# Kernel optimization log

Hardware: AMD Instinct MI355X
Metric: run time of the kernel (lower is better)

The kernel has to match this reference:

```python
import jax, jax.numpy as jnp
import numpy as np

QLEN, MLEN, D, H = 1024, 1024, 1024, 16
DH = D // H
KLEN = QLEN + MLEN
SCALE = 1.0 / np.sqrt(DH).astype(np.float32)
W_STD = 0.02


def setup_inputs() -> dict:
    key = jax.random.key(0)
    ks = jax.random.split(key, 14)
    inputs = jax.random.normal(ks[0], (QLEN, 1, D), jnp.float32)
    r = jax.random.normal(ks[1], (KLEN, D), jnp.float32)
    u = jax.random.normal(ks[2], (H, DH), jnp.float32) * W_STD
    v = jax.random.normal(ks[3], (H, DH), jnp.float32) * W_STD
    mem = jax.random.normal(ks[4], (MLEN, 1, D), jnp.float32)
    # causal mask over concatenated [mem, inputs] keys: True = masked
    attn_mask = jnp.triu(jnp.ones((QLEN, KLEN), bool), k=MLEN + 1)
    W_qkv = jax.random.normal(ks[5], (3 * D, D), jnp.float32) * W_STD
    W_r = jax.random.normal(ks[6], (D, D), jnp.float32) * W_STD
    W_o = jax.random.normal(ks[7], (D, D), jnp.float32) * W_STD
    W_ih = jax.random.normal(ks[8], (3 * D, D), jnp.float32) * W_STD
    W_hh = jax.random.normal(ks[9], (3 * D, D), jnp.float32) * W_STD
    b_ih = jnp.zeros((3 * D,), jnp.float32)
    b_hh = jnp.zeros((3 * D,), jnp.float32)
    h0 = jnp.zeros((1, 1, D), jnp.float32)  # GRU hidden, forces batch=1
    return {"inputs": inputs, "r": r, "u": u, "v": v, "attn_mask": attn_mask,
            "mem": mem, "W_qkv": W_qkv, "W_r": W_r, "W_o": W_o,
            "W_ih": W_ih, "W_hh": W_hh, "b_ih": b_ih, "b_hh": b_hh, "h0": h0}


def _rel_shift(x):
    # Transformer-XL relative shift; x: [qlen, klen, b, n]
    q, k, b, n = x.shape
    zp = jnp.zeros((q, 1, b, n), x.dtype)
    xp = jnp.concatenate([zp, x], axis=1)          # [q, k+1, b, n]
    xp = xp.reshape(k + 1, q, b, n)[1:]            # drop first row
    return xp.reshape(q, k, b, n)


def reference(inputs, r, u, v, attn_mask, mem, W_qkv, W_r, W_o,
              W_ih, W_hh, b_ih, b_hh, h0):
    qlen, b, d = inputs.shape
    cat = jnp.concatenate([mem, inputs], axis=0)        # [klen, b, d]
    klen = cat.shape[0]
    w_heads = cat @ W_qkv.T                             # [klen, b, 3d]
    q_h, k_h, v_h = jnp.split(w_heads, 3, axis=-1)
    q_h = q_h[-qlen:].reshape(qlen, b, H, DH)
    k_h = k_h.reshape(klen, b, H, DH)
    v_h = v_h.reshape(klen, b, H, DH)
    r_k = (r @ W_r.T).reshape(klen, H, DH)              # relative key heads

    AC = jnp.einsum('ibnd,jbnd->ijbn', q_h + u, k_h)    # content score
    BD = _rel_shift(jnp.einsum('ibnd,jnd->ijbn', q_h + v, r_k))  # position score
    score = (AC + BD) * SCALE                           # [q, k, b, n]
    score = jnp.where(attn_mask[:, :, None, None], jnp.float32(-1e30), score)
    probs = jax.nn.softmax(score, axis=1)

    attn_vec = jnp.einsum('ijbn,jbnd->ibnd', probs, v_h).reshape(qlen, b, d)
    y = attn_vec @ W_o.T                                # [q, b, d]

    # 1-layer GRU over time (PyTorch gate order r, z, n)
    x_proj = y @ W_ih.T + b_ih                          # [q, b, 3d]

    def step(h, xt):
        gh = h @ W_hh.T + b_hh
        xr, xz, xn = jnp.split(xt, 3, axis=-1)
        hr, hz, hn = jnp.split(gh, 3, axis=-1)
        rg = jax.nn.sigmoid(xr + hr)
        zg = jax.nn.sigmoid(xz + hz)
        ng = jnp.tanh(xn + rg * hn)
        h_new = (1.0 - zg) * ng + zg * h
        return h_new, h_new

    _, ys = jax.lax.scan(step, h0[0], x_proj)           # h0[0]: [b, d]
    return ys, probs
```

## Files before the change

### kernel.cpp

```cpp
#include <hip/hip_runtime.h>
#include <hip/hip_bf16.h>
#include <math.h>

#define QL   1024
#define ML   1024
#define KL   2048
#define DM   1024
#define NH   16
#define DH   64
#define SCL  0.125f
#define GRU_BLOCKS 128
#define GRU_ELPB   8

typedef __attribute__((ext_vector_type(8))) short bfrag;
typedef __attribute__((ext_vector_type(4))) float facc;

static __device__ __forceinline__ float dot4(const float4& a, const float4& b) {
    return a.x*b.x + a.y*b.y + a.z*b.z + a.w*b.w;
}

static __device__ __forceinline__ unsigned bf16_rne(float x) {
    unsigned u = __float_as_uint(x);
    return (u + 0x7FFF + ((u >> 16) & 1)) >> 16;
}
static __device__ __forceinline__ void bfsplit(float a, short& h, short& l) {
    unsigned uh = bf16_rne(a);
    h = (short)uh;
    float ah = __uint_as_float(uh << 16);
    l = (short)bf16_rne(a - ah);
}

__global__ __launch_bounds__(256) void gemm_nt_mfma(
    const float* __restrict__ A, const float* __restrict__ B,
    const float* __restrict__ bias, float* __restrict__ C,
    int M, int N, int K, int skipM, int skipN)
{
    const int bx = blockIdx.x, by = blockIdx.y;
    if (by < skipM && bx < skipN) return;
    __shared__ short Ah[128*40], Al[128*40], Bh[128*40], Bl[128*40];
    const int tid = threadIdx.x;
    const int wv = tid >> 6, ln = tid & 63;
    const int wr = wv >> 1, wc = wv & 1;
    const int lm = ln & 15, lk = ln >> 4;
    facc acc[4][4] = {};

    const int srow = tid >> 1;
    const int scol = (tid & 1) << 4;
    const float* Ap = A + (size_t)(by*128 + srow)*K + scol;
    const float* Bp = B + (size_t)(bx*128 + srow)*K + scol;

    float4 ar[4], br[4];
    #pragma unroll
    for (int c = 0; c < 4; c++) {
        ar[c] = *(const float4*)(Ap + c*4);
        br[c] = *(const float4*)(Bp + c*4);
    }

    for (int k0 = 0; k0 < K; k0 += 32) {
        bfrag a_h0, a_h1, a_l0, a_l1, b_h0, b_h1, b_l0, b_l1;
        #pragma unroll
        for (int c = 0; c < 4; c++) {
            const float av[4] = {ar[c].x, ar[c].y, ar[c].z, ar[c].w};
            const float bv[4] = {br[c].x, br[c].y, br[c].z, br[c].w};
            #pragma unroll
            for (int q = 0; q < 4; q++) {
                const int e = c*4 + q;
                short h, l;
                bfsplit(av[q], h, l);
                if (e < 8) { a_h0[e] = h; a_l0[e] = l; }
                else       { a_h1[e-8] = h; a_l1[e-8] = l; }
                bfsplit(bv[q], h, l);
                if (e < 8) { b_h0[e] = h; b_l0[e] = l; }
                else       { b_h1[e-8] = h; b_l1[e-8] = l; }
            }
        }
        __syncthreads();
        *(bfrag*)&Ah[srow*40 + scol    ] = a_h0;
        *(bfrag*)&Ah[srow*40 + scol + 8] = a_h1;
        *(bfrag*)&Al[srow*40 + scol    ] = a_l0;
        *(bfrag*)&Al[srow*40 + scol + 8] = a_l1;
        *(bfrag*)&Bh[srow*40 + scol    ] = b_h0;
        *(bfrag*)&Bh[srow*40 + scol + 8] = b_h1;
        *(bfrag*)&Bl[srow*40 + scol    ] = b_l0;
        *(bfrag*)&Bl[srow*40 + scol + 8] = b_l1;
        __syncthreads();
        if (k0 + 32 < K) {
            #pragma unroll
            for (int c = 0; c < 4; c++) {
                ar[c] = *(const float4*)(Ap + k0 + 32 + c*4);
                br[c] = *(const float4*)(Bp + k0 + 32 + c*4);
            }
        }
        bfrag fah[4], fal[4], fbh[4], fbl[4];
        #pragma unroll
        for (int i = 0; i < 4; i++) {
            const int rA = wr*64 + i*16 + lm;
            fah[i] = *(const bfrag*)&Ah[rA*40 + lk*8];
            fal[i] = *(const bfrag*)&Al[rA*40 + lk*8];
            const int rB = wc*64 + i*16 + lm;
            fbh[i] = *(const bfrag*)&Bh[rB*40 + lk*8];
            fbl[i] = *(const bfrag*)&Bl[rB*40 + lk*8];
        }
        #pragma unroll
        for (int i = 0; i < 4; i++)
            #pragma unroll
            for (int j = 0; j < 4; j++) {
                acc[i][j] = __builtin_amdgcn_mfma_f32_16x16x32_bf16(fah[i], fbh[j], acc[i][j], 0, 0, 0);
                acc[i][j] = __builtin_amdgcn_mfma_f32_16x16x32_bf16(fah[i], fbl[j], acc[i][j], 0, 0, 0);
                acc[i][j] = __builtin_amdgcn_mfma_f32_16x16x32_bf16(fal[i], fbh[j], acc[i][j], 0, 0, 0);
            }
    }

    const int m0 = by*128 + wr*64 + lk*4;
    const int n0 = bx*128 + wc*64 + lm;
    #pragma unroll
    for (int j = 0; j < 4; j++) {
        const float bj = bias ? bias[n0 + j*16] : 0.f;
        #pragma unroll
        for (int i = 0; i < 4; i++)
            #pragma unroll
            for (int r = 0; r < 4; r++)
                C[(size_t)(m0 + i*16 + r)*N + n0 + j*16] = acc[i][j][r] + bj;
    }
}

__global__ __launch_bounds__(256) void wd_kernel(
    const float* __restrict__ rk, const float* __restrict__ u_,
    const float* __restrict__ v_, float* __restrict__ wd)
{
    int idx = blockIdx.x*256 + threadIdx.x;
    if (idx >= NH*KL) return;
    int n = idx >> 11, jr = idx & (KL-1);
    const float* rp = rk + (size_t)jr*DM + n*DH;
    const float* up = u_ + n*DH;
    const float* vp = v_ + n*DH;
    float s = 0.f;
    #pragma unroll
    for (int d4 = 0; d4 < 16; d4++) {
        float4 r4 = *(const float4*)(rp + d4*4);
        float4 uu = *(const float4*)(up + d4*4);
        float4 vv = *(const float4*)(vp + d4*4);
        s += (vv.x-uu.x)*r4.x + (vv.y-uu.y)*r4.y + (vv.z-uu.z)*r4.z + (vv.w-uu.w)*r4.w;
    }
    wd[idx] = s;
}

__global__ __launch_bounds__(256) void score_kernel(
    const float* __restrict__ wh, const float* __restrict__ rk,
    const float* __restrict__ u_, const float* __restrict__ wd,
    float* __restrict__ sc)
{
    const int jt = blockIdx.x, it = blockIdx.y, n = blockIdx.z;
    const int i0 = it*64, j0 = jt*64;
    if (j0 > i0 + 1087) return;
    __shared__ float squ[64*64];
    __shared__ float sk [64*64];
    __shared__ float sr [128*64];
    __shared__ float swd[128];
    const int tid = threadIdx.x;
    #pragma unroll
    for (int rr = 0; rr < 4; rr++) {
        int p = tid + 256*rr;
        int row = p >> 4, c4 = p & 15;
        int phys = (c4 ^ ((row >> 2) & 15)) << 2;
        float4 q4 = *(const float4*)&wh[(size_t)(ML + i0 + row)*3072 + n*DH + (c4<<2)];
        float4 u4 = *(const float4*)&u_[n*DH + (c4<<2)];
        float4 t4; t4.x=q4.x+u4.x; t4.y=q4.y+u4.y; t4.z=q4.z+u4.z; t4.w=q4.w+u4.w;
        *(float4*)&squ[row*64 + phys] = t4;
        float4 k4 = *(const float4*)&wh[(size_t)(j0 + row)*3072 + DM + n*DH + (c4<<2)];
        *(float4*)&sk[row*64 + phys] = k4;
    }
    const int jr0 = j0 - i0 + 960;
    #pragma unroll
    for (int rr = 0; rr < 8; rr++) {
        int p = tid + 256*rr;
        int row = p >> 4, c4 = p & 15;
        int phys = (c4 ^ ((row >> 2) & 15)) << 2;
        int jr = jr0 + row;
        float4 r4;
        if (jr >= 0 && jr < KL) r4 = *(const float4*)&rk[(size_t)jr*DM + n*DH + (c4<<2)];
        else { r4.x = r4.y = r4.z = r4.w = 0.f; }
        *(float4*)&sr[row*64 + phys] = r4;
    }
    if (tid < 128) {
        int jr = jr0 + tid;
        swd[tid] = (jr >= 0 && jr < KL) ? wd[n*KL + jr] : 0.f;
    }
    __syncthreads();

    const int tj2 = tid & 15, ti2 = tid >> 4;
    const int rbase = tj2*4 - ti2*4 + 60;
    float acc[4][4] = {};
    #pragma unroll
    for (int dc = 0; dc < 16; dc++) {
        float4 qa[4], kb[4], rv[7];
        #pragma unroll
        for (int a = 0; a < 4; a++) {
            int row = ti2*4 + a;
            qa[a] = *(const float4*)&squ[row*64 + ((dc ^ ((row>>2)&15)) << 2)];
        }
        #pragma unroll
        for (int b_ = 0; b_ < 4; b_++) {
            int row = tj2*4 + b_;
            kb[b_] = *(const float4*)&sk[row*64 + ((dc ^ ((row>>2)&15)) << 2)];
        }
        #pragma unroll
        for (int o = 0; o < 7; o++) {
            int row = rbase + o;
            rv[o] = *(const float4*)&sr[row*64 + ((dc ^ ((row>>2)&15)) << 2)];
        }
        #pragma unroll
        for (int a = 0; a < 4; a++)
            #pragma unroll
            for (int b_ = 0; b_ < 4; b_++)
                acc[a][b_] += dot4(qa[a], kb[b_]) + dot4(qa[a], rv[3 + b_ - a]);
    }
    #pragma unroll
    for (int a = 0; a < 4; a++) {
        int i = i0 + ti2*4 + a;
        float4 o;
        o.x = (acc[a][0] + swd[rbase + 3 + 0 - a]) * SCL;
        o.y = (acc[a][1] + swd[rbase + 3 + 1 - a]) * SCL;
        o.z = (acc[a][2] + swd[rbase + 3 + 2 - a]) * SCL;
        o.w = (acc[a][3] + swd[rbase + 3 + 3 - a]) * SCL;
        *(float4*)&sc[((size_t)i*NH + n)*KL + j0 + (tj2<<2)] = o;
    }
}

__global__ __launch_bounds__(512) void softmaxT_kernel(float* __restrict__ sc)
{
    const int i = blockIdx.x;
    const int tid = threadIdx.x;
    __shared__ float ld[16*2052];
    __shared__ float sinv[16];
    float* slab = sc + (size_t)i*KL*NH;
    #pragma unroll
    for (int rr = 0; rr < 16; rr++) {
        int p = tid + 512*rr;
        int nn = p >> 9, j = (p & 511) << 2;
        float4 f = *(const float4*)(slab + ((size_t)nn << 11) + j);
        *(float4*)&ld[nn*2052 + j] = f;
    }
    __syncthreads();
    const int g = tid >> 5, tl = tid & 31;
    const int jmax = i + ML;
    float m = -3.4e38f;
    for (int k = 0; k < 64; k++) {
        int j = tl + (k << 5);
        if (j <= jmax) m = fmaxf(m, ld[g*2052 + j]);
    }
    #pragma unroll
    for (int off = 1; off <= 16; off <<= 1) m = fmaxf(m, __shfl_xor(m, off, 64));
    float ssum = 0.f;
    for (int k = 0; k < 64; k++) {
        int j = tl + (k << 5);
        float e = 0.f;
        if (j <= jmax) { e = __expf(ld[g*2052 + j] - m); ssum += e; }
        ld[g*2052 + j] = e;
    }
    #pragma unroll
    for (int off = 1; off <= 16; off <<= 1) ssum += __shfl_xor(ssum, off, 64);
    if (tl == 0) sinv[g] = 1.f / ssum;
    __syncthreads();
    #pragma unroll
    for (int rr = 0; rr < 16; rr++) {
        int p = tid + 512*rr;
        int j = p >> 2, n0 = (p & 3) << 2;
        float4 o;
        o.x = ld[(n0+0)*2052 + j] * sinv[n0+0];
        o.y = ld[(n0+1)*2052 + j] * sinv[n0+1];
        o.z = ld[(n0+2)*2052 + j] * sinv[n0+2];
        o.w = ld[(n0+3)*2052 + j] * sinv[n0+3];
        *(float4*)(slab + (size_t)p*4) = o;
    }
}

__global__ __launch_bounds__(512) void pv_kernel(
    const float* __restrict__ sc, const float* __restrict__ wh,
    float* __restrict__ attn)
{
    const int it = blockIdx.x >> 1, dh = blockIdx.x & 1;
    const int i0 = it*8;
    const int tid = threadIdx.x;
    __shared__ float Ps[8*16*20];
    __shared__ float Vs[16][512];
    const int col = dh*512 + tid;
    const int nn = col >> 6;
    float acc[8] = {};
    const int jlast = i0 + 7 + ML;
    const int nch = (jlast + 16) >> 4;
    for (int ch = 0; ch < nch; ch++) {
        const int j0 = ch << 4;
        __syncthreads();
        {
            int ii = tid >> 6, rem = tid & 63, jj = rem >> 2, n0 = (rem & 3) << 2;
            float4 f = *(const float4*)(sc + ((size_t)(i0+ii)*KL + j0 + jj)*NH + n0);
            Ps[(ii*16 + n0+0)*20 + jj] = f.x;
            Ps[(ii*16 + n0+1)*20 + jj] = f.y;
            Ps[(ii*16 + n0+2)*20 + jj] = f.z;
            Ps[(ii*16 + n0+3)*20 + jj] = f.w;
        }
        #pragma unroll
        for (int rr = 0; rr < 4; rr++) {
            int p = tid + 512*rr;
            int row = p >> 7, c4 = (p & 127) << 2;
            float4 f = *(const float4*)&wh[(size_t)(j0+row)*3072 + 2048 + dh*512 + c4];
            *(float4*)&Vs[row][c4] = f;
        }
        __syncthreads();
        #pragma unroll
        for (int jq = 0; jq < 4; jq++) {
            float4 pv[8];
            #pragma unroll
            for (int ii = 0; ii < 8; ii++)
                pv[ii] = *(const float4*)&Ps[(ii*16 + nn)*20 + jq*4];
            #pragma unroll
            for (int jj = 0; jj < 4; jj++) {
                float vv = Vs[jq*4 + jj][tid];
                #pragma unroll
                for (int ii = 0; ii < 8; ii++)
                    acc[ii] += ((const float*)&pv[ii])[jj] * vv;
            }
        }
    }
    #pragma unroll
    for (int ii = 0; ii < 8; ii++)
        attn[(size_t)(i0+ii)*DM + col] = acc[ii];
}

__global__ __launch_bounds__(512) void gru_persistent(
    const float* __restrict__ xp,
    const float* __restrict__ Whh,
    const float* __restrict__ bhh,
    const float* __restrict__ h0,
    float* __restrict__ ys,
    unsigned long long* __restrict__ hpack)
{
    __shared__ float wlds[3][GRU_ELPB][DM];
    __shared__ float hlds[DM];
    const int b = blockIdx.x;
    const int tid = threadIdx.x;
    const int w = tid >> 6, l = tid & 63;
    const int dg = b*GRU_ELPB + w;

    #pragma unroll
    for (int k = 0; k < 12; k++) {
        int idx = tid + 512*k;
        int g   = idx >> 11;
        int rem = idx & 2047;
        int e   = rem >> 8;
        int c   = rem & 255;
        float4 f = *(const float4*)&Whh[(size_t)(g*DM + b*GRU_ELPB + e)*DM + (c<<2)];
        *(float4*)&wlds[g][e][c<<2] = f;
    }
    float bh0=0.f, bh1=0.f, bh2=0.f, hreg=0.f;
    if (l == 0) {
        bh0 = bhh[dg]; bh1 = bhh[dg + DM]; bh2 = bhh[dg + 2*DM];
        hreg = h0[dg];
    }

    bool bail = false;
    for (int t = 0; t < QL; t++) {
        float xr=0.f, xz=0.f, xn=0.f;
        if (l == 0) {
            const float* xrow = xp + (size_t)t*3072 + dg;
            xr = xrow[0]; xz = xrow[DM]; xn = xrow[2*DM];
        }
        if (t == 0) {
            hlds[tid]       = h0[tid];
            hlds[tid + 512] = h0[tid + 512];
        } else if (!bail) {
            const unsigned long long* hp = hpack + ((size_t)(t & 1) << 10);
            #define GRU_LDA(i) __hip_atomic_load(&hp[tid + (i)*512], \
                __ATOMIC_RELAXED, __HIP_MEMORY_SCOPE_AGENT)
            unsigned long long a0 = GRU_LDA(0), b0 = GRU_LDA(1);
            unsigned long long a1 = GRU_LDA(0), b1 = GRU_LDA(1);
            unsigned long long a2 = GRU_LDA(0), b2 = GRU_LDA(1);
            unsigned long long v0, v1;
            int guard = 0;
            for (;;) {
                if ((unsigned)(a0 >> 32) >= (unsigned)t &&
                    (unsigned)(b0 >> 32) >= (unsigned)t) { v0 = a0; v1 = b0; break; }
                a0 = a1; b0 = b1;
                a1 = a2; b1 = b2;
                a2 = GRU_LDA(0); b2 = GRU_LDA(1);
                if (++guard > (1<<18)) { bail = true; v0 = GRU_LDA(0); v1 = GRU_LDA(1); break; }
            }
            #undef GRU_LDA
            hlds[tid]       = __uint_as_float((unsigned)v0);
            hlds[tid + 512] = __uint_as_float((unsigned)v1);
        }
        __syncthreads();

        float s0=0.f, s1=0.f, s2=0.f;
        #pragma unroll
        for (int c = 0; c < 4; c++) {
            const int base = c*256 + l*4;
            float4 h4 = *(const float4*)&hlds[base];
            float4 w0 = *(const float4*)&wlds[0][w][base];
            float4 w1 = *(const float4*)&wlds[1][w][base];
            float4 w2 = *(const float4*)&wlds[2][w][base];
            s0 += dot4(w0, h4);
            s1 += dot4(w1, h4);
            s2 += dot4(w2, h4);
        }
        #pragma unroll
        for (int off = 32; off >= 1; off >>= 1) {
            s0 += __shfl_xor(s0, off, 64);
            s1 += __shfl_xor(s1, off, 64);
            s2 += __shfl_xor(s2, off, 64);
        }
        if (l == 0) {
            const float hr = s0 + bh0;
            const float hz = s1 + bh1;
            const float hn = s2 + bh2;
            const float rg = 1.f/(1.f + __expf(-(xr + hr)));
            const float zg = 1.f/(1.f + __expf(-(xz + hz)));
            const float e2 = __expf(2.f*(xn + rg*hn));
            const float ng = (e2 - 1.f) / (e2 + 1.f);
            const float hnew = (1.f - zg)*ng + zg*hreg;
            hreg = hnew;
            unsigned long long pk = (unsigned long long)__float_as_uint(hnew)
                                  | ((unsigned long long)(unsigned)(t+1) << 32);
            __hip_atomic_store(&hpack[(((size_t)(t+1) & 1) << 10) + dg], pk,
                               __ATOMIC_RELAXED, __HIP_MEMORY_SCOPE_AGENT);
            ys[(size_t)t*DM + dg] = hnew;
        }
    }
}

extern "C" void kernel_launch(void* const* d_in, const int* in_sizes, int n_in,
                              void* d_out, int out_size, void* d_ws, size_t ws_size,
                              hipStream_t stream) {
    const float* inputs = (const float*)d_in[0];
    const float* r_in   = (const float*)d_in[1];
    const float* u_in   = (const float*)d_in[2];
    const float* v_in   = (const float*)d_in[3];
    const float* mem    = (const float*)d_in[5];
    const float* Wqkv   = (const float*)d_in[6];
    const float* Wr     = (const float*)d_in[7];
    const float* Wo     = (const float*)d_in[8];
    const float* Wih    = (const float*)d_in[9];
    const float* Whh    = (const float*)d_in[10];
    const float* b_ih   = (const float*)d_in[11];
    const float* b_hh   = (const float*)d_in[12];
    const float* h0     = (const float*)d_in[13];

    float* out = (float*)d_out;
    float* ys  = out;
    float* sc  = out + (size_t)QL*DM;

    float* ws      = (float*)d_ws;
    float* cat     = ws;
    float* wheads  = cat    + (size_t)KL*DM;
    float* rk      = wheads + (size_t)KL*3072;
    float* wd      = rk     + (size_t)KL*DM;
    float* attn    = wd     + (size_t)NH*KL;
    float* ybuf    = attn   + (size_t)QL*DM;
    float* xproj   = ybuf   + (size_t)QL*DM;
    unsigned long long* hpack = (unsigned long long*)(xproj + (size_t)QL*3072);

    hipMemcpyAsync(cat,            mem,    (size_t)ML*DM*4, hipMemcpyDeviceToDevice, stream);
    hipMemcpyAsync(cat + (size_t)ML*DM, inputs, (size_t)QL*DM*4, hipMemcpyDeviceToDevice, stream);
    hipMemsetAsync(hpack, 0, 2*DM*sizeof(unsigned long long), stream);

    gemm_nt_mfma<<<dim3(24,16), 256, 0, stream>>>(cat, Wqkv, nullptr, wheads, KL, 3072, DM, 8, 8);
    gemm_nt_mfma<<<dim3(8,16), 256, 0, stream>>>(r_in, Wr, nullptr, rk, KL, DM, DM, 0, 0);
    wd_kernel<<<128, 256, 0, stream>>>(rk, u_in, v_in, wd);
    score_kernel<<<dim3(32,16,16), 256, 0, stream>>>(wheads, rk, u_in, wd, sc);
    softmaxT_kernel<<<QL, 512, 0, stream>>>(sc);
    pv_kernel<<<256, 512, 0, stream>>>(sc, wheads, attn);
    gemm_nt_mfma<<<dim3(8,8), 256, 0, stream>>>(attn, Wo, nullptr, ybuf, QL, DM, DM, 0, 0);
    gemm_nt_mfma<<<dim3(24,8), 256, 0, stream>>>(ybuf, Wih, b_ih, xproj, QL, 3072, DM, 0, 0);
    gru_persistent<<<GRU_BLOCKS, 512, 0, stream>>>(xproj, Whh, b_hh, h0, ys, hpack);
}
```

Before: 2.892 ms.

## Keep GRU recurrent weights in registers and halve persistent block count

The persistent GRU kernel now holds each wave's slice of W_hh in VGPRs (two hidden elements per wave, six rows) instead of LDS, and runs 64 blocks of 16 elements instead of 128 blocks of 8. The aim is to cut the LDS weight reads on every timestep and to have fewer blocks taking part in the cross-block spin-wait handoff. The spin loop now polls each half independently rather than through a pipelined triple buffer, and a second __syncthreads is added per step to protect hlds reuse. The risks are register pressure from the 96 weight floats per thread and serial gate math on lane 0 that now covers twice as many elements.

```diff
diff --git a/kernel.cpp b/kernel.cpp
--- a/kernel.cpp
+++ b/kernel.cpp
@@ -9,8 +9,8 @@
 #define NH   16
 #define DH   64
 #define SCL  0.125f
-#define GRU_BLOCKS 128
-#define GRU_ELPB   8
+#define GRU_BLOCKS 64
+#define GRU_ELPB   16
 
 typedef __attribute__((ext_vector_type(8))) short bfrag;
 typedef __attribute__((ext_vector_type(4))) float facc;
@@ -328,7 +328,7 @@
         attn[(size_t)(i0+ii)*DM + col] = acc[ii];
 }
 
-__global__ __launch_bounds__(512) void gru_persistent(
+__global__ __launch_bounds__(512, 2) void gru_persistent(
     const float* __restrict__ xp,
     const float* __restrict__ Whh,
     const float* __restrict__ bhh,
@@ -336,96 +336,110 @@
     float* __restrict__ ys,
     unsigned long long* __restrict__ hpack)
 {
-    __shared__ float wlds[3][GRU_ELPB][DM];
     __shared__ float hlds[DM];
     const int b = blockIdx.x;
     const int tid = threadIdx.x;
     const int w = tid >> 6, l = tid & 63;
-    const int dg = b*GRU_ELPB + w;
-
-    #pragma unroll
-    for (int k = 0; k < 12; k++) {
-        int idx = tid + 512*k;
-        int g   = idx >> 11;
-        int rem = idx & 2047;
-        int e   = rem >> 8;
-        int c   = rem & 255;
-        float4 f = *(const float4*)&Whh[(size_t)(g*DM + b*GRU_ELPB + e)*DM + (c<<2)];
-        *(float4*)&wlds[g][e][c<<2] = f;
-    }
-    float bh0=0.f, bh1=0.f, bh2=0.f, hreg=0.f;
+    const int e0 = b*GRU_ELPB + 2*w;
+
+    float wt[6][16];
+    #pragma unroll
+    for (int ee = 0; ee < 2; ee++)
+        #pragma unroll
+        for (int g = 0; g < 3; g++) {
+            const float* src = Whh + (size_t)(g*DM + e0 + ee)*DM;
+            const int k = ee*3 + g;
+            #pragma unroll
+            for (int c = 0; c < 4; c++) {
+                float4 f = *(const float4*)(src + c*256 + l*4);
+                wt[k][c*4+0]=f.x; wt[k][c*4+1]=f.y; wt[k][c*4+2]=f.z; wt[k][c*4+3]=f.w;
+            }
+        }
+    #pragma unroll
+    for (int k = 0; k < 6; k++)
+        #pragma unroll
+        for (int c = 0; c < 16; c++)
+            asm volatile("" : "+v"(wt[k][c]));
+
+    float bh[6] = {0,0,0,0,0,0};
+    float hreg0 = 0.f, hreg1 = 0.f;
     if (l == 0) {
-        bh0 = bhh[dg]; bh1 = bhh[dg + DM]; bh2 = bhh[dg + 2*DM];
-        hreg = h0[dg];
+        #pragma unroll
+        for (int ee = 0; ee < 2; ee++)
+            #pragma unroll
+            for (int g = 0; g < 3; g++)
+                bh[ee*3+g] = bhh[g*DM + e0 + ee];
+        hreg0 = h0[e0]; hreg1 = h0[e0 + 1];
     }
 
     bool bail = false;
     for (int t = 0; t < QL; t++) {
-        float xr=0.f, xz=0.f, xn=0.f;
+        float xv[6] = {0,0,0,0,0,0};
         if (l == 0) {
-            const float* xrow = xp + (size_t)t*3072 + dg;
-            xr = xrow[0]; xz = xrow[DM]; xn = xrow[2*DM];
+            const float* xrow = xp + (size_t)t*3072 + e0;
+            #pragma unroll
+            for (int ee = 0; ee < 2; ee++)
+                #pragma unroll
+                for (int g = 0; g < 3; g++)
+                    xv[ee*3+g] = xrow[g*DM + ee];
         }
         if (t == 0) {
             hlds[tid]       = h0[tid];
             hlds[tid + 512] = h0[tid + 512];
         } else if (!bail) {
             const unsigned long long* hp = hpack + ((size_t)(t & 1) << 10);
-            #define GRU_LDA(i) __hip_atomic_load(&hp[tid + (i)*512], \
-                __ATOMIC_RELAXED, __HIP_MEMORY_SCOPE_AGENT)
-            unsigned long long a0 = GRU_LDA(0), b0 = GRU_LDA(1);
-            unsigned long long a1 = GRU_LDA(0), b1 = GRU_LDA(1);
-            unsigned long long a2 = GRU_LDA(0), b2 = GRU_LDA(1);
-            unsigned long long v0, v1;
+            unsigned long long v0 = 0, v1 = 0;
+            bool d0 = false, d1 = false;
             int guard = 0;
             for (;;) {
-                if ((unsigned)(a0 >> 32) >= (unsigned)t &&
-                    (unsigned)(b0 >> 32) >= (unsigned)t) { v0 = a0; v1 = b0; break; }
-                a0 = a1; b0 = b1;
-                a1 = a2; b1 = b2;
-                a2 = GRU_LDA(0); b2 = GRU_LDA(1);
-                if (++guard > (1<<18)) { bail = true; v0 = GRU_LDA(0); v1 = GRU_LDA(1); break; }
-            }
-            #undef GRU_LDA
+                if (!d0) { v0 = __hip_atomic_load(&hp[tid],       __ATOMIC_RELAXED, __HIP_MEMORY_SCOPE_AGENT);
+                           d0 = (unsigned)(v0 >> 32) >= (unsigned)t; }
+                if (!d1) { v1 = __hip_atomic_load(&hp[tid + 512], __ATOMIC_RELAXED, __HIP_MEMORY_SCOPE_AGENT);
+                           d1 = (unsigned)(v1 >> 32) >= (unsigned)t; }
+                if (d0 && d1) break;
+                if (++guard > (1<<18)) { bail = true; break; }
+            }
             hlds[tid]       = __uint_as_float((unsigned)v0);
             hlds[tid + 512] = __uint_as_float((unsigned)v1);
         }
         __syncthreads();
 
-        float s0=0.f, s1=0.f, s2=0.f;
+        float s[6] = {0,0,0,0,0,0};
         #pragma unroll
         for (int c = 0; c < 4; c++) {
-            const int base = c*256 + l*4;
-            float4 h4 = *(const float4*)&hlds[base];
-            float4 w0 = *(const float4*)&wlds[0][w][base];
-            float4 w1 = *(const float4*)&wlds[1][w][base];
-            float4 w2 = *(const float4*)&wlds[2][w][base];
-            s0 += dot4(w0, h4);
-            s1 += dot4(w1, h4);
-            s2 += dot4(w2, h4);
-        }
-        #pragma unroll
-        for (int off = 32; off >= 1; off >>= 1) {
-            s0 += __shfl_xor(s0, off, 64);
-            s1 += __shfl_xor(s1, off, 64);
-            s2 += __shfl_xor(s2, off, 64);
-        }
+            float4 h4 = *(const float4*)&hlds[c*256 + l*4];
+            #pragma unroll
+            for (int k = 0; k < 6; k++) {
+                s[k] += wt[k][c*4+0]*h4.x + wt[k][c*4+1]*h4.y
+                      + wt[k][c*4+2]*h4.z + wt[k][c*4+3]*h4.w;
+            }
+        }
+        #pragma unroll
+        for (int k = 0; k < 6; k++)
+            #pragma unroll
+            for (int off = 32; off >= 1; off >>= 1)
+                s[k] += __shfl_xor(s[k], off, 64);
         if (l == 0) {
-            const float hr = s0 + bh0;
-            const float hz = s1 + bh1;
-            const float hn = s2 + bh2;
-            const float rg = 1.f/(1.f + __expf(-(xr + hr)));
-            const float zg = 1.f/(1.f + __expf(-(xz + hz)));
-            const float e2 = __expf(2.f*(xn + rg*hn));
-            const float ng = (e2 - 1.f) / (e2 + 1.f);
-            const float hnew = (1.f - zg)*ng + zg*hreg;
-            hreg = hnew;
-            unsigned long long pk = (unsigned long long)__float_as_uint(hnew)
-                                  | ((unsigned long long)(unsigned)(t+1) << 32);
-            __hip_atomic_store(&hpack[(((size_t)(t+1) & 1) << 10) + dg], pk,
-                               __ATOMIC_RELAXED, __HIP_MEMORY_SCOPE_AGENT);
-            ys[(size_t)t*DM + dg] = hnew;
-        }
+            #pragma unroll
+            for (int ee = 0; ee < 2; ee++) {
+                const float hr = s[ee*3+0] + bh[ee*3+0];
+                const float hz = s[ee*3+1] + bh[ee*3+1];
+                const float hn = s[ee*3+2] + bh[ee*3+2];
+                const float hold = ee ? hreg1 : hreg0;
+                const float rg = 1.f/(1.f + __expf(-(xv[ee*3+0] + hr)));
+                const float zg = 1.f/(1.f + __expf(-(xv[ee*3+1] + hz)));
+                const float e2 = __expf(2.f*(xv[ee*3+2] + rg*hn));
+                const float ng = (e2 - 1.f) / (e2 + 1.f);
+                const float hnew = (1.f - zg)*ng + zg*hold;
+                if (ee) hreg1 = hnew; else hreg0 = hnew;
+                unsigned long long pk = (unsigned long long)__float_as_uint(hnew)
+                                      | ((unsigned long long)(unsigned)(t+1) << 32);
+                __hip_atomic_store(&hpack[(((size_t)(t+1) & 1) << 10) + e0 + ee], pk,
+                                   __ATOMIC_RELAXED, __HIP_MEMORY_SCOPE_AGENT);
+                ys[(size_t)t*DM + e0 + ee] = hnew;
+            }
+        }
+        __syncthreads();
     }
 }
 
```

Result: slower. 3.651 ms (+26.3%).
